# Kernel tuning notes

Measured on AMD Instinct MI355X. Metric: run time of the kernel, lower is better.

The kernel has to match this reference:

```python
import jax, jax.numpy as jnp
import numpy as np

IN, HID, OUT = 64, 256, 64
B, NSTEPS, DELAY = 256, 1024, 20


def setup_inputs() -> dict:
    key = jax.random.key(0)
    ks = jax.random.split(key, 8)
    s = 0.05
    return {
        "input": jax.random.normal(ks[0], (B, NSTEPS, IN), jnp.float32),
        "W_ih_x": jax.random.normal(ks[1], (4 * HID, IN), jnp.float32) * s,
        "W_ih_fb": jax.random.normal(ks[2], (4 * HID, OUT), jnp.float32) * s,
        "W_hh": jax.random.normal(ks[3], (4 * HID, HID), jnp.float32) * s,
        "b_ih": jax.random.normal(ks[4], (4 * HID,), jnp.float32) * s,
        "b_hh": jax.random.normal(ks[5], (4 * HID,), jnp.float32) * s,
        "W_out": jax.random.normal(ks[6], (OUT, HID), jnp.float32) * s,
        "b_out": jax.random.normal(ks[7], (OUT,), jnp.float32) * s,
        "delay": DELAY,
    }


def reference(input, W_ih_x, W_ih_fb, W_hh, b_ih, b_hh, W_out, b_out, delay):
    b, nsteps, _ = input.shape
    H = W_hh.shape[1]
    O = W_out.shape[0]
    # Precompute the input contribution to the gates for all timesteps:
    # gates_t = x_t @ W_ih_x.T + fb @ W_ih_fb.T + h @ W_hh.T + b_ih + b_hh
    xg = jnp.einsum("btd,gd->tbg", input, W_ih_x) + (b_ih + b_hh)  # [T, B, 4H]

    h0 = jnp.zeros((b, H), input.dtype)
    c0 = jnp.zeros((b, H), input.dtype)
    buf0 = jnp.zeros((delay, b, O), input.dtype)  # ring buffer of past outputs
    ptr0 = jnp.zeros((), jnp.int32)

    def step(carry, xg_t):
        h, c, buf, ptr = carry
        fb = buf[ptr]  # output from `delay` steps ago (zeros initially)
        gates = xg_t + fb @ W_ih_fb.T + h @ W_hh.T  # [B, 4H]
        i, f, g, o = jnp.split(gates, 4, axis=-1)  # torch LSTMCell gate order
        c = jax.nn.sigmoid(f) * c + jax.nn.sigmoid(i) * jnp.tanh(g)
        h = jax.nn.sigmoid(o) * jnp.tanh(c)
        out = h @ W_out.T + b_out  # [B, O]
        buf = buf.at[ptr].set(out)
        ptr = (ptr + 1) % delay
        return (h, c, buf, ptr), out

    _, outs = jax.lax.scan(step, (h0, c0, buf0, ptr0), xg)  # outs: [T, B, O]
    return jnp.transpose(outs, (1, 0, 2))  # [B, T, O]
```

## Files before the change

### kernel.cpp

```cpp
#include <hip/hip_runtime.h>


#define BATCH   256
#define TSTEPS  1024
#define IN_DIM  64
#define HID     256
#define OUT_DIM 64
#define DELAY   20
#define CH      8
#define NCH     (TSTEPS / CH)
#define NTHR    512
#define REGV    10
#define AGP     15

typedef unsigned int u32;
typedef _Float16 half2_t __attribute__((ext_vector_type(2)));

union H2U { u32 u; half2_t h; };
union H1U { unsigned short s; _Float16 h; };

__device__ __forceinline__ u32 pack2(float a, float b) {
    H2U x; x.h = half2_t{(_Float16)a, (_Float16)b}; return x.u;
}
__device__ __forceinline__ unsigned short f16bits(float a) {
    H1U x; x.h = (_Float16)a; return x.s;
}
__device__ __forceinline__ float lo16(u32 u) {
    H1U x; x.s = (unsigned short)(u & 0xffffu); return (float)x.h;
}
__device__ __forceinline__ float hi16(u32 u) {
    H1U x; x.s = (unsigned short)(u >> 16); return (float)x.h;
}
__device__ __forceinline__ float dot2(u32 w, u32 h, float acc) {
    H2U a; a.u = w; H2U b; b.u = h;
    return __builtin_amdgcn_fdot2(a.h, b.h, acc, false);
}
__device__ __forceinline__ float sigm(float x) {
    float e = __expf(-fabsf(x));
    float p = 1.f / (1.f + e);
    return x >= 0.f ? p : 1.f - p;
}
__device__ __forceinline__ float tanh_f(float x) {
    float e = __expf(-2.f * fabsf(x));
    float r = (1.f - e) / (1.f + e);
    return x >= 0.f ? r : -r;
}

#define AGWRITE(dst, src) \
    asm volatile("v_accvgpr_write_b32 %0, %1" : "=a"(dst) : "v"(src))
#define AGREAD(dst, src) \
    asm volatile("v_accvgpr_read_b32 %0, %1" : "=v"(dst) : "a"(src))

#define OFF_WA    0
#define OFF_WB    65536
#define OFF_WC    98304
#define OFF_CB    114688
#define OFF_PART  131072
#define OFF_RING  139264
#define OFF_XF    141824
#define OFF_HG    144000
#define SMEM_BYTES 152192

#define WS_BPK   0
#define WS_WOUT  262144
#define WS_BSUM  294912
#define WS_NEED  299008

__device__ __forceinline__ int orig_row(int gp) {
    return (gp & 3) * 256 + (gp >> 2);
}

__global__ void prepack(const float* __restrict__ Wx,
                        const float* __restrict__ Wfb,
                        const float* __restrict__ Whh,
                        const float* __restrict__ Wout,
                        const float* __restrict__ bih,
                        const float* __restrict__ bhh,
                        uint4* __restrict__ Bpk4,
                        u32* __restrict__ Woutpk,
                        float* __restrict__ bsum_g)
{
    (void)Whh;
    int id = blockIdx.x * 256 + threadIdx.x;
    if (id < 16384) {
        int t = id & 511, rest = id >> 9;
        int kb = rest & 15, j = rest >> 4;
        int r = orig_row(2 * t + j);
        int k0 = kb * 8;
        const float* src = (k0 < 64) ? (Wx + (size_t)r * 64 + k0)
                                     : (Wfb + (size_t)r * 64 + (k0 - 64));
        uint4 v;
        v.x = pack2(src[0], src[1]); v.y = pack2(src[2], src[3]);
        v.z = pack2(src[4], src[5]); v.w = pack2(src[6], src[7]);
        Bpk4[id] = v;
    } else if (id < 16384 + 8192) {
        int s = id - 16384;
        int c = s & 3, o = (s >> 2) & 63, w4 = s >> 8;
        int kp = w4 * 4 + c;
        Woutpk[s] = pack2(Wout[o * HID + 2 * kp], Wout[o * HID + 2 * kp + 1]);
    } else if (id < 16384 + 8192 + 1024) {
        int g = id - 24576;
        int r = orig_row(g);
        bsum_g[g] = bih[r] + bhh[r];
    }
}

__global__ __attribute__((amdgpu_flat_work_group_size(NTHR, NTHR)))
__attribute__((amdgpu_waves_per_eu(2, 2)))
void lstm_persist(const float* __restrict__ input,
                  const float* __restrict__ Whh,
                  const float* __restrict__ bout_g,
                  const uint4* __restrict__ Bpk4,
                  const u32* __restrict__ Woutpk,
                  const float* __restrict__ bsum_g,
                  float* __restrict__ out)
{
    __shared__ alignas(16) unsigned char smem[SMEM_BYTES];
    uint4*          wAl   = (uint4*)(smem + OFF_WA);
    uint2*          wBl   = (uint2*)(smem + OFF_WB);
    u32*            wCl   = (u32*)(smem + OFF_WC);
    u32*            cb32  = (u32*)(smem + OFF_CB);
    unsigned short* part  = (unsigned short*)(smem + OFF_PART);
    unsigned short* ring  = (unsigned short*)(smem + OFF_RING);
    u32*            xfst  = (u32*)(smem + OFF_XF);
    unsigned short* hgs   = (unsigned short*)(smem + OFF_HG);

    const int tid = threadIdx.x;
    const int b   = blockIdx.x;
    const int kq  = tid >> 7;
    const int gl  = tid & 127;

    const float* xin  = input + (size_t)b * TSTEPS * IN_DIM;
    float*       outp = out + (size_t)b * TSTEPS * OUT_DIM;
    const float bo_reg = bout_g[tid & 63];

    u32 wregv[8][REGV];
    u32 wag[8][AGP];
#pragma unroll
    for (int q = 0; q < 8; ++q) {
        const int r = orig_row(gl * 8 + q);
        const float* wrow = Whh + (size_t)r * HID + kq * 64;
#pragma unroll
        for (int p = 0; p < REGV; ++p) {
            float2 w2 = *(const float2*)(wrow + 2 * p);
            wregv[q][p] = pack2(w2.x, w2.y);
        }
        uint4 av;
        av.x = pack2(wrow[20], wrow[21]); av.y = pack2(wrow[22], wrow[23]);
        av.z = pack2(wrow[24], wrow[25]); av.w = pack2(wrow[26], wrow[27]);
        wAl[q * 512 + tid] = av;
        uint2 bv;
        bv.x = pack2(wrow[28], wrow[29]); bv.y = pack2(wrow[30], wrow[31]);
        wBl[q * 512 + tid] = bv;
        wCl[q * 512 + tid] = pack2(wrow[32], wrow[33]);
#pragma unroll
        for (int j = 0; j < AGP; ++j) {
            float2 w2 = *(const float2*)(wrow + 34 + 2 * j);
            u32 v = pack2(w2.x, w2.y);
            AGWRITE(wag[q][j], v);
        }
    }
    {
        u32* hz = (u32*)hgs;
        hz[tid] = 0u; hz[512 + tid] = 0u; hz[1024 + tid] = 0u; hz[1536 + tid] = 0u;
    }
    __syncthreads();

    float c_state = 0.f;

    auto out_chunk = [&](int tbase) {
        const int lt = tid >> 6, o = tid & 63;
        const int t = tbase + lt;
        const uint4* hrow = (const uint4*)(hgs + (t & 15) * HID);
        const uint4* wp = (const uint4*)Woutpk;
        float a = bo_reg;
        for (int w4 = 0; w4 < 32; ++w4) {
            uint4 wv = wp[w4 * 64 + o];
            uint4 hv = hrow[w4];
            a = dot2(wv.x, hv.x, a); a = dot2(wv.y, hv.y, a);
            a = dot2(wv.z, hv.z, a); a = dot2(wv.w, hv.w, a);
        }
        outp[(size_t)t * OUT_DIM + o] = a;
        ring[(t % DELAY) * 64 + o] = f16bits(a);
    };

#pragma unroll 1
    for (int ch = 0; ch < NCH; ++ch) {
#pragma unroll
        for (int q = 0; q < 8; ++q) {
#pragma unroll
            for (int p = 0; p < REGV; ++p)
                asm volatile("" : "+v"(wregv[q][p]));
#pragma unroll
            for (int j = 0; j < AGP; ++j)
                asm volatile("" : "+a"(wag[q][j]));
        }

        const int t0 = ch * CH;
        if (ch > 0) out_chunk(t0 - CH);
        __syncthreads();

        {
            int row = tid >> 6, p = tid & 63;
            int t = t0 + row;
            u32 v;
            if (p < 32) {
                float2 x2 = *(const float2*)(xin + (size_t)t * IN_DIM + 2 * p);
                v = pack2(x2.x, x2.y);
            } else {
                int src = t - DELAY;
                if (src >= 0) {
                    int d = 2 * (p - 32);
                    int sl = src % DELAY;
                    v = (u32)ring[sl * 64 + d] | ((u32)ring[sl * 64 + d + 1] << 16);
                } else v = 0u;
            }
            xfst[row * 68 + p] = v;
        }
        __syncthreads();

        {
            float accA[8], accB[8];
#pragma unroll
            for (int i = 0; i < 8; ++i) { accA[i] = 0.f; accB[i] = 0.f; }
            const uint4* bA = Bpk4 + tid;
            const uint4* bB = Bpk4 + 16 * 512 + tid;
#pragma unroll 1
            for (int kb = 0; kb < 16; ++kb) {
                uint4 wA = bA[kb * 512];
                uint4 wB = bB[kb * 512];
#pragma unroll
                for (int tl = 0; tl < 8; ++tl) {
                    uint4 xv = *(const uint4*)(xfst + tl * 68 + kb * 4);
                    accA[tl] = dot2(wA.x, xv.x, accA[tl]);
                    accA[tl] = dot2(wA.y, xv.y, accA[tl]);
                    accA[tl] = dot2(wA.z, xv.z, accA[tl]);
                    accA[tl] = dot2(wA.w, xv.w, accA[tl]);
                    accB[tl] = dot2(wB.x, xv.x, accB[tl]);
                    accB[tl] = dot2(wB.y, xv.y, accB[tl]);
                    accB[tl] = dot2(wB.z, xv.z, accB[tl]);
                    accB[tl] = dot2(wB.w, xv.w, accB[tl]);
                }
            }
            float2 bs = *(const float2*)(bsum_g + 2 * tid);
#pragma unroll
            for (int tl = 0; tl < 8; ++tl)
                cb32[tl * 512 + tid] = pack2(accA[tl] + bs.x, accB[tl] + bs.y);
        }
        __syncthreads();

#pragma unroll 1
        for (int tl = 0; tl < CH; ++tl) {
            const int t = t0 + tl;
            const u32* hrow = (const u32*)hgs + ((t - 1) & 15) * 128 + kq * 32;

            float acc[8];
            if (kq == 0) {
                uint4 cv = *(const uint4*)(cb32 + tl * 512 + gl * 4);
                acc[0] = lo16(cv.x); acc[1] = hi16(cv.x);
                acc[2] = lo16(cv.y); acc[3] = hi16(cv.y);
                acc[4] = lo16(cv.z); acc[5] = hi16(cv.z);
                acc[6] = lo16(cv.w); acc[7] = hi16(cv.w);
            } else {
#pragma unroll
                for (int q = 0; q < 8; ++q) acc[q] = 0.f;
            }
            {
                uint4 h0 = *(const uint4*)(hrow + 0);
                uint4 h1 = *(const uint4*)(hrow + 4);
                uint4 h2 = *(const uint4*)(hrow + 8);
                uint4 h3 = *(const uint4*)(hrow + 12);
#pragma unroll
                for (int q = 0; q < 8; ++q) {
                    acc[q] = dot2(wregv[q][0], h0.x, acc[q]);
                    acc[q] = dot2(wregv[q][1], h0.y, acc[q]);
                    acc[q] = dot2(wregv[q][2], h0.z, acc[q]);
                    acc[q] = dot2(wregv[q][3], h0.w, acc[q]);
                    acc[q] = dot2(wregv[q][4], h1.x, acc[q]);
                    acc[q] = dot2(wregv[q][5], h1.y, acc[q]);
                    acc[q] = dot2(wregv[q][6], h1.z, acc[q]);
                    acc[q] = dot2(wregv[q][7], h1.w, acc[q]);
                    acc[q] = dot2(wregv[q][8], h2.x, acc[q]);
                    acc[q] = dot2(wregv[q][9], h2.y, acc[q]);
                    uint4 av = wAl[q * 512 + tid];
                    uint2 bv = wBl[q * 512 + tid];
                    acc[q] = dot2(av.x, h2.z, acc[q]);
                    acc[q] = dot2(av.y, h2.w, acc[q]);
                    acc[q] = dot2(av.z, h3.x, acc[q]);
                    acc[q] = dot2(av.w, h3.y, acc[q]);
                    acc[q] = dot2(bv.x, h3.z, acc[q]);
                    acc[q] = dot2(bv.y, h3.w, acc[q]);
                }
            }
            {
                uint4 h4 = *(const uint4*)(hrow + 16);
                uint4 h5 = *(const uint4*)(hrow + 20);
                uint4 h6 = *(const uint4*)(hrow + 24);
                uint4 h7 = *(const uint4*)(hrow + 28);
#pragma unroll
                for (int q = 0; q < 8; ++q) {
                    u32 cv = wCl[q * 512 + tid];
                    acc[q] = dot2(cv, h4.x, acc[q]);
                    u32 t0r, t1r, t2r, t3r;
                    AGREAD(t0r, wag[q][0]);  acc[q] = dot2(t0r, h4.y, acc[q]);
                    AGREAD(t1r, wag[q][1]);  acc[q] = dot2(t1r, h4.z, acc[q]);
                    AGREAD(t2r, wag[q][2]);  acc[q] = dot2(t2r, h4.w, acc[q]);
                    AGREAD(t3r, wag[q][3]);  acc[q] = dot2(t3r, h5.x, acc[q]);
                    AGREAD(t0r, wag[q][4]);  acc[q] = dot2(t0r, h5.y, acc[q]);
                    AGREAD(t1r, wag[q][5]);  acc[q] = dot2(t1r, h5.z, acc[q]);
                    AGREAD(t2r, wag[q][6]);  acc[q] = dot2(t2r, h5.w, acc[q]);
                    AGREAD(t3r, wag[q][7]);  acc[q] = dot2(t3r, h6.x, acc[q]);
                    AGREAD(t0r, wag[q][8]);  acc[q] = dot2(t0r, h6.y, acc[q]);
                    AGREAD(t1r, wag[q][9]);  acc[q] = dot2(t1r, h6.z, acc[q]);
                    AGREAD(t2r, wag[q][10]); acc[q] = dot2(t2r, h6.w, acc[q]);
                    AGREAD(t3r, wag[q][11]); acc[q] = dot2(t3r, h7.x, acc[q]);
                    AGREAD(t0r, wag[q][12]); acc[q] = dot2(t0r, h7.y, acc[q]);
                    AGREAD(t1r, wag[q][13]); acc[q] = dot2(t1r, h7.z, acc[q]);
                    AGREAD(t2r, wag[q][14]); acc[q] = dot2(t2r, h7.w, acc[q]);
                }
            }
            {
                uint4 pw;
                pw.x = pack2(acc[0], acc[1]); pw.y = pack2(acc[2], acc[3]);
                pw.z = pack2(acc[4], acc[5]); pw.w = pack2(acc[6], acc[7]);
                *(uint4*)(part + kq * 1024 + gl * 8) = pw;
            }
            __syncthreads();

            if (tid < 256) {
                float s0 = 0.f, s1 = 0.f, s2 = 0.f, s3 = 0.f;
#pragma unroll
                for (int k = 0; k < 4; ++k) {
                    uint2 rd = *(const uint2*)(part + k * 1024 + tid * 4);
                    s0 += lo16(rd.x); s1 += hi16(rd.x);
                    s2 += lo16(rd.y); s3 += hi16(rd.y);
                }
                c_state = sigm(s1) * c_state + sigm(s0) * tanh_f(s2);
                float hval = sigm(s3) * tanh_f(c_state);
                hgs[(t & 15) * HID + tid] = f16bits(hval);
            }
            __syncthreads();
        }
    }
    out_chunk(TSTEPS - CH);
}

extern "C" void kernel_launch(void* const* d_in, const int* in_sizes, int n_in,
                              void* d_out, int out_size, void* d_ws, size_t ws_size,
                              hipStream_t stream)
{
    (void)in_sizes; (void)n_in; (void)out_size;
    const float* input = (const float*)d_in[0];
    const float* Wx    = (const float*)d_in[1];
    const float* Wfb   = (const float*)d_in[2];
    const float* Whh   = (const float*)d_in[3];
    const float* bih   = (const float*)d_in[4];
    const float* bhh   = (const float*)d_in[5];
    const float* Wo    = (const float*)d_in[6];
    const float* bog   = (const float*)d_in[7];
    float* out = (float*)d_out;

    if (ws_size < (size_t)WS_NEED) return;

    uint4* Bpk4   = (uint4*)((char*)d_ws + WS_BPK);
    u32*   Woutpk = (u32*)((char*)d_ws + WS_WOUT);
    float* bsum_g = (float*)((char*)d_ws + WS_BSUM);

    prepack<<<dim3(100), dim3(256), 0, stream>>>(
        Wx, Wfb, Whh, Wo, bih, bhh, Bpk4, Woutpk, bsum_g);
    lstm_persist<<<dim3(BATCH), dim3(NTHR), 0, stream>>>(
        input, Whh, bog, Bpk4, Woutpk, bsum_g, out);
}
```

Measured before the change: 5.194 ms.

## Assign each hidden unit's four gates to a lane pair and reduce via shuffle

The recurrent matvec is remapped so that each pair of adjacent threads owns all four gates of one hidden unit, with each lane covering half of the K dimension. Previously each thread covered 8 gate rows over a quarter of K. The cross-K reduction now uses a wavefront shuffle, so the LDS partial-sum buffer, one __syncthreads per timestep and the serial gate stage on half the threads all go away. Each lane also splits its dot products across two accumulators for more instruction-level parallelism. In exchange both lanes compute the cell update redundantly, and the weight split across VGPRs, AGPRs and LDS changes, using slightly more LDS.

```diff
diff --git a/kernel.cpp b/kernel.cpp
--- a/kernel.cpp
+++ b/kernel.cpp
@@ -10,8 +10,6 @@
 #define CH      8
 #define NCH     (TSTEPS / CH)
 #define NTHR    512
-#define REGV    10
-#define AGP     15
 
 typedef unsigned int u32;
 typedef _Float16 half2_t __attribute__((ext_vector_type(2)));
@@ -51,15 +49,12 @@
 #define AGREAD(dst, src) \
     asm volatile("v_accvgpr_read_b32 %0, %1" : "=v"(dst) : "a"(src))
 
-#define OFF_WA    0
-#define OFF_WB    65536
-#define OFF_WC    98304
-#define OFF_CB    114688
-#define OFF_PART  131072
-#define OFF_RING  139264
-#define OFF_XF    141824
-#define OFF_HG    144000
-#define SMEM_BYTES 152192
+#define OFF_WL    0
+#define OFF_CB    131072
+#define OFF_RING  147456
+#define OFF_XF    150016
+#define OFF_HG    152192
+#define SMEM_BYTES 160384
 
 #define WS_BPK   0
 #define WS_WOUT  262144
@@ -116,48 +111,45 @@
                   float* __restrict__ out)
 {
     __shared__ alignas(16) unsigned char smem[SMEM_BYTES];
-    uint4*          wAl   = (uint4*)(smem + OFF_WA);
-    uint2*          wBl   = (uint2*)(smem + OFF_WB);
-    u32*            wCl   = (u32*)(smem + OFF_WC);
+    uint4*          wl4   = (uint4*)(smem + OFF_WL);
     u32*            cb32  = (u32*)(smem + OFF_CB);
-    unsigned short* part  = (unsigned short*)(smem + OFF_PART);
     unsigned short* ring  = (unsigned short*)(smem + OFF_RING);
     u32*            xfst  = (u32*)(smem + OFF_XF);
     unsigned short* hgs   = (unsigned short*)(smem + OFF_HG);
 
     const int tid = threadIdx.x;
     const int b   = blockIdx.x;
-    const int kq  = tid >> 7;
-    const int gl  = tid & 127;
+    const int u   = tid >> 1;
+    const int kh  = tid & 1;
 
     const float* xin  = input + (size_t)b * TSTEPS * IN_DIM;
     float*       outp = out + (size_t)b * TSTEPS * OUT_DIM;
     const float bo_reg = bout_g[tid & 63];
 
-    u32 wregv[8][REGV];
-    u32 wag[8][AGP];
-#pragma unroll
-    for (int q = 0; q < 8; ++q) {
-        const int r = orig_row(gl * 8 + q);
-        const float* wrow = Whh + (size_t)r * HID + kq * 64;
-#pragma unroll
-        for (int p = 0; p < REGV; ++p) {
+    u32 wregv[4][18];
+    u32 wag[4][30];
+#pragma unroll
+    for (int j = 0; j < 4; ++j) {
+        const int r = j * 256 + u;
+        const float* wrow = Whh + (size_t)r * HID + kh * 128;
+#pragma unroll
+        for (int p = 0; p < 18; ++p) {
             float2 w2 = *(const float2*)(wrow + 2 * p);
-            wregv[q][p] = pack2(w2.x, w2.y);
-        }
-        uint4 av;
-        av.x = pack2(wrow[20], wrow[21]); av.y = pack2(wrow[22], wrow[23]);
-        av.z = pack2(wrow[24], wrow[25]); av.w = pack2(wrow[26], wrow[27]);
-        wAl[q * 512 + tid] = av;
-        uint2 bv;
-        bv.x = pack2(wrow[28], wrow[29]); bv.y = pack2(wrow[30], wrow[31]);
-        wBl[q * 512 + tid] = bv;
-        wCl[q * 512 + tid] = pack2(wrow[32], wrow[33]);
-#pragma unroll
-        for (int j = 0; j < AGP; ++j) {
-            float2 w2 = *(const float2*)(wrow + 34 + 2 * j);
+            wregv[j][p] = pack2(w2.x, w2.y);
+        }
+#pragma unroll
+        for (int p = 0; p < 30; ++p) {
+            float2 w2 = *(const float2*)(wrow + 36 + 2 * p);
             u32 v = pack2(w2.x, w2.y);
-            AGWRITE(wag[q][j], v);
+            AGWRITE(wag[j][p], v);
+        }
+#pragma unroll
+        for (int pp = 0; pp < 4; ++pp) {
+            const float* w = wrow + 96 + 8 * pp;
+            uint4 v;
+            v.x = pack2(w[0], w[1]); v.y = pack2(w[2], w[3]);
+            v.z = pack2(w[4], w[5]); v.w = pack2(w[6], w[7]);
+            wl4[(j * 4 + pp) * 512 + tid] = v;
         }
     }
     {
@@ -187,13 +179,13 @@
 #pragma unroll 1
     for (int ch = 0; ch < NCH; ++ch) {
 #pragma unroll
-        for (int q = 0; q < 8; ++q) {
-#pragma unroll
-            for (int p = 0; p < REGV; ++p)
-                asm volatile("" : "+v"(wregv[q][p]));
-#pragma unroll
-            for (int j = 0; j < AGP; ++j)
-                asm volatile("" : "+a"(wag[q][j]));
+        for (int j = 0; j < 4; ++j) {
+#pragma unroll
+            for (int p = 0; p < 18; ++p)
+                asm volatile("" : "+v"(wregv[j][p]));
+#pragma unroll
+            for (int p = 0; p < 30; ++p)
+                asm volatile("" : "+a"(wag[j][p]));
         }
 
         const int t0 = ch * CH;
@@ -252,44 +244,43 @@
 #pragma unroll 1
         for (int tl = 0; tl < CH; ++tl) {
             const int t = t0 + tl;
-            const u32* hrow = (const u32*)hgs + ((t - 1) & 15) * 128 + kq * 32;
-
-            float acc[8];
-            if (kq == 0) {
-                uint4 cv = *(const uint4*)(cb32 + tl * 512 + gl * 4);
+            const u32* hrow = (const u32*)hgs + ((t - 1) & 15) * 128 + kh * 64;
+
+            float acc[4], ac2[4];
+            if (kh == 0) {
+                uint2 cv = *(const uint2*)(cb32 + tl * 512 + 2 * u);
                 acc[0] = lo16(cv.x); acc[1] = hi16(cv.x);
                 acc[2] = lo16(cv.y); acc[3] = hi16(cv.y);
-                acc[4] = lo16(cv.z); acc[5] = hi16(cv.z);
-                acc[6] = lo16(cv.w); acc[7] = hi16(cv.w);
             } else {
 #pragma unroll
-                for (int q = 0; q < 8; ++q) acc[q] = 0.f;
-            }
+                for (int j = 0; j < 4; ++j) acc[j] = 0.f;
+            }
+#pragma unroll
+            for (int j = 0; j < 4; ++j) ac2[j] = 0.f;
+
             {
                 uint4 h0 = *(const uint4*)(hrow + 0);
                 uint4 h1 = *(const uint4*)(hrow + 4);
                 uint4 h2 = *(const uint4*)(hrow + 8);
                 uint4 h3 = *(const uint4*)(hrow + 12);
 #pragma unroll
-                for (int q = 0; q < 8; ++q) {
-                    acc[q] = dot2(wregv[q][0], h0.x, acc[q]);
-                    acc[q] = dot2(wregv[q][1], h0.y, acc[q]);
-                    acc[q] = dot2(wregv[q][2], h0.z, acc[q]);
-                    acc[q] = dot2(wregv[q][3], h0.w, acc[q]);
-                    acc[q] = dot2(wregv[q][4], h1.x, acc[q]);
-                    acc[q] = dot2(wregv[q][5], h1.y, acc[q]);
-                    acc[q] = dot2(wregv[q][6], h1.z, acc[q]);
-                    acc[q] = dot2(wregv[q][7], h1.w, acc[q]);
-                    acc[q] = dot2(wregv[q][8], h2.x, acc[q]);
-                    acc[q] = dot2(wregv[q][9], h2.y, acc[q]);
-                    uint4 av = wAl[q * 512 + tid];
-                    uint2 bv = wBl[q * 512 + tid];
-                    acc[q] = dot2(av.x, h2.z, acc[q]);
-                    acc[q] = dot2(av.y, h2.w, acc[q]);
-                    acc[q] = dot2(av.z, h3.x, acc[q]);
-                    acc[q] = dot2(av.w, h3.y, acc[q]);
-                    acc[q] = dot2(bv.x, h3.z, acc[q]);
-                    acc[q] = dot2(bv.y, h3.w, acc[q]);
+                for (int j = 0; j < 4; ++j) {
+                    acc[j] = dot2(wregv[j][0], h0.x, acc[j]);
+                    ac2[j] = dot2(wregv[j][1], h0.y, ac2[j]);
+                    acc[j] = dot2(wregv[j][2], h0.z, acc[j]);
+                    ac2[j] = dot2(wregv[j][3], h0.w, ac2[j]);
+                    acc[j] = dot2(wregv[j][4], h1.x, acc[j]);
+                    ac2[j] = dot2(wregv[j][5], h1.y, ac2[j]);
+                    acc[j] = dot2(wregv[j][6], h1.z, acc[j]);
+                    ac2[j] = dot2(wregv[j][7], h1.w, ac2[j]);
+                    acc[j] = dot2(wregv[j][8], h2.x, acc[j]);
+                    ac2[j] = dot2(wregv[j][9], h2.y, ac2[j]);
+                    acc[j] = dot2(wregv[j][10], h2.z, acc[j]);
+                    ac2[j] = dot2(wregv[j][11], h2.w, ac2[j]);
+                    acc[j] = dot2(wregv[j][12], h3.x, acc[j]);
+                    ac2[j] = dot2(wregv[j][13], h3.y, ac2[j]);
+                    acc[j] = dot2(wregv[j][14], h3.z, acc[j]);
+                    ac2[j] = dot2(wregv[j][15], h3.w, ac2[j]);
                 }
             }
             {
@@ -298,46 +289,110 @@
                 uint4 h6 = *(const uint4*)(hrow + 24);
                 uint4 h7 = *(const uint4*)(hrow + 28);
 #pragma unroll
-                for (int q = 0; q < 8; ++q) {
-                    u32 cv = wCl[q * 512 + tid];
-                    acc[q] = dot2(cv, h4.x, acc[q]);
-                    u32 t0r, t1r, t2r, t3r;
-                    AGREAD(t0r, wag[q][0]);  acc[q] = dot2(t0r, h4.y, acc[q]);
-                    AGREAD(t1r, wag[q][1]);  acc[q] = dot2(t1r, h4.z, acc[q]);
-                    AGREAD(t2r, wag[q][2]);  acc[q] = dot2(t2r, h4.w, acc[q]);
-                    AGREAD(t3r, wag[q][3]);  acc[q] = dot2(t3r, h5.x, acc[q]);
-                    AGREAD(t0r, wag[q][4]);  acc[q] = dot2(t0r, h5.y, acc[q]);
-                    AGREAD(t1r, wag[q][5]);  acc[q] = dot2(t1r, h5.z, acc[q]);
-                    AGREAD(t2r, wag[q][6]);  acc[q] = dot2(t2r, h5.w, acc[q]);
-                    AGREAD(t3r, wag[q][7]);  acc[q] = dot2(t3r, h6.x, acc[q]);
-                    AGREAD(t0r, wag[q][8]);  acc[q] = dot2(t0r, h6.y, acc[q]);
-                    AGREAD(t1r, wag[q][9]);  acc[q] = dot2(t1r, h6.z, acc[q]);
-                    AGREAD(t2r, wag[q][10]); acc[q] = dot2(t2r, h6.w, acc[q]);
-                    AGREAD(t3r, wag[q][11]); acc[q] = dot2(t3r, h7.x, acc[q]);
-                    AGREAD(t0r, wag[q][12]); acc[q] = dot2(t0r, h7.y, acc[q]);
-                    AGREAD(t1r, wag[q][13]); acc[q] = dot2(t1r, h7.z, acc[q]);
-                    AGREAD(t2r, wag[q][14]); acc[q] = dot2(t2r, h7.w, acc[q]);
+                for (int j = 0; j < 4; ++j) {
+                    acc[j] = dot2(wregv[j][16], h4.x, acc[j]);
+                    ac2[j] = dot2(wregv[j][17], h4.y, ac2[j]);
+                    u32 w0, w1, w2, w3;
+                    AGREAD(w0, wag[j][0]); AGREAD(w1, wag[j][1]);
+                    AGREAD(w2, wag[j][2]); AGREAD(w3, wag[j][3]);
+                    acc[j] = dot2(w0, h4.z, acc[j]);
+                    ac2[j] = dot2(w1, h4.w, ac2[j]);
+                    acc[j] = dot2(w2, h5.x, acc[j]);
+                    ac2[j] = dot2(w3, h5.y, ac2[j]);
+                    AGREAD(w0, wag[j][4]); AGREAD(w1, wag[j][5]);
+                    AGREAD(w2, wag[j][6]); AGREAD(w3, wag[j][7]);
+                    acc[j] = dot2(w0, h5.z, acc[j]);
+                    ac2[j] = dot2(w1, h5.w, ac2[j]);
+                    acc[j] = dot2(w2, h6.x, acc[j]);
+                    ac2[j] = dot2(w3, h6.y, ac2[j]);
+                    AGREAD(w0, wag[j][8]); AGREAD(w1, wag[j][9]);
+                    AGREAD(w2, wag[j][10]); AGREAD(w3, wag[j][11]);
+                    acc[j] = dot2(w0, h6.z, acc[j]);
+                    ac2[j] = dot2(w1, h6.w, ac2[j]);
+                    acc[j] = dot2(w2, h7.x, acc[j]);
+                    ac2[j] = dot2(w3, h7.y, ac2[j]);
+                    AGREAD(w0, wag[j][12]); AGREAD(w1, wag[j][13]);
+                    acc[j] = dot2(w0, h7.z, acc[j]);
+                    ac2[j] = dot2(w1, h7.w, ac2[j]);
                 }
             }
             {
-                uint4 pw;
-                pw.x = pack2(acc[0], acc[1]); pw.y = pack2(acc[2], acc[3]);
-                pw.z = pack2(acc[4], acc[5]); pw.w = pack2(acc[6], acc[7]);
-                *(uint4*)(part + kq * 1024 + gl * 8) = pw;
-            }
-            __syncthreads();
-
-            if (tid < 256) {
-                float s0 = 0.f, s1 = 0.f, s2 = 0.f, s3 = 0.f;
-#pragma unroll
-                for (int k = 0; k < 4; ++k) {
-                    uint2 rd = *(const uint2*)(part + k * 1024 + tid * 4);
-                    s0 += lo16(rd.x); s1 += hi16(rd.x);
-                    s2 += lo16(rd.y); s3 += hi16(rd.y);
+                uint4 h8 = *(const uint4*)(hrow + 32);
+                uint4 h9 = *(const uint4*)(hrow + 36);
+                uint4 ha = *(const uint4*)(hrow + 40);
+                uint4 hb = *(const uint4*)(hrow + 44);
+#pragma unroll
+                for (int j = 0; j < 4; ++j) {
+                    u32 w0, w1, w2, w3;
+                    AGREAD(w0, wag[j][14]); AGREAD(w1, wag[j][15]);
+                    AGREAD(w2, wag[j][16]); AGREAD(w3, wag[j][17]);
+                    acc[j] = dot2(w0, h8.x, acc[j]);
+                    ac2[j] = dot2(w1, h8.y, ac2[j]);
+                    acc[j] = dot2(w2, h8.z, acc[j]);
+                    ac2[j] = dot2(w3, h8.w, ac2[j]);
+                    AGREAD(w0, wag[j][18]); AGREAD(w1, wag[j][19]);
+                    AGREAD(w2, wag[j][20]); AGREAD(w3, wag[j][21]);
+                    acc[j] = dot2(w0, h9.x, acc[j]);
+                    ac2[j] = dot2(w1, h9.y, ac2[j]);
+                    acc[j] = dot2(w2, h9.z, acc[j]);
+                    ac2[j] = dot2(w3, h9.w, ac2[j]);
+                    AGREAD(w0, wag[j][22]); AGREAD(w1, wag[j][23]);
+                    AGREAD(w2, wag[j][24]); AGREAD(w3, wag[j][25]);
+                    acc[j] = dot2(w0, ha.x, acc[j]);
+                    ac2[j] = dot2(w1, ha.y, ac2[j]);
+                    acc[j] = dot2(w2, ha.z, acc[j]);
+                    ac2[j] = dot2(w3, ha.w, ac2[j]);
+                    AGREAD(w0, wag[j][26]); AGREAD(w1, wag[j][27]);
+                    AGREAD(w2, wag[j][28]); AGREAD(w3, wag[j][29]);
+                    acc[j] = dot2(w0, hb.x, acc[j]);
+                    ac2[j] = dot2(w1, hb.y, ac2[j]);
+                    acc[j] = dot2(w2, hb.z, acc[j]);
+                    ac2[j] = dot2(w3, hb.w, ac2[j]);
                 }
-                c_state = sigm(s1) * c_state + sigm(s0) * tanh_f(s2);
-                float hval = sigm(s3) * tanh_f(c_state);
-                hgs[(t & 15) * HID + tid] = f16bits(hval);
+            }
+            {
+                uint4 hc = *(const uint4*)(hrow + 48);
+                uint4 hd = *(const uint4*)(hrow + 52);
+                uint4 he = *(const uint4*)(hrow + 56);
+                uint4 hf = *(const uint4*)(hrow + 60);
+#pragma unroll
+                for (int j = 0; j < 4; ++j) {
+                    uint4 v0 = wl4[(j * 4 + 0) * 512 + tid];
+                    uint4 v1 = wl4[(j * 4 + 1) * 512 + tid];
+                    uint4 v2 = wl4[(j * 4 + 2) * 512 + tid];
+                    uint4 v3 = wl4[(j * 4 + 3) * 512 + tid];
+                    acc[j] = dot2(v0.x, hc.x, acc[j]);
+                    ac2[j] = dot2(v0.y, hc.y, ac2[j]);
+                    acc[j] = dot2(v0.z, hc.z, acc[j]);
+                    ac2[j] = dot2(v0.w, hc.w, ac2[j]);
+                    acc[j] = dot2(v1.x, hd.x, acc[j]);
+                    ac2[j] = dot2(v1.y, hd.y, ac2[j]);
+                    acc[j] = dot2(v1.z, hd.z, acc[j]);
+                    ac2[j] = dot2(v1.w, hd.w, ac2[j]);
+                    acc[j] = dot2(v2.x, he.x, acc[j]);
+                    ac2[j] = dot2(v2.y, he.y, ac2[j]);
+                    acc[j] = dot2(v2.z, he.z, acc[j]);
+                    ac2[j] = dot2(v2.w, he.w, ac2[j]);
+                    acc[j] = dot2(v3.x, hf.x, acc[j]);
+                    ac2[j] = dot2(v3.y, hf.y, ac2[j]);
+                    acc[j] = dot2(v3.z, hf.z, acc[j]);
+                    ac2[j] = dot2(v3.w, hf.w, ac2[j]);
+                }
+            }
+
+            {
+                u32 pa = pack2(acc[0] + ac2[0], acc[1] + ac2[1]);
+                u32 pb = pack2(acc[2] + ac2[2], acc[3] + ac2[3]);
+                u32 qa = (u32)__shfl_xor((int)pa, 1, 64);
+                u32 qb = (u32)__shfl_xor((int)pb, 1, 64);
+                float Si = lo16(pa) + lo16(qa);
+                float Sf = hi16(pa) + hi16(qa);
+                float Sg = lo16(pb) + lo16(qb);
+                float So = hi16(pb) + hi16(qb);
+                c_state = sigm(Sf) * c_state + sigm(Si) * tanh_f(Sg);
+                float hval = sigm(So) * tanh_f(c_state);
+                if (kh == 0)
+                    hgs[(t & 15) * HID + u] = f16bits(hval);
             }
             __syncthreads();
         }
```

Result: faster. 5.079 ms (-2.2%).
